# Performance work log

Measured on AMD Instinct MI355X. Metric: run time of the kernel, lower is better.

## Reference

```python
import jax, jax.numpy as jnp
import numpy as np

B, S, HIDDEN, H, HD = 4, 1024, 1024, 16, 64  # head_dim = hidden/heads; rel-pos 'd_model' = HD
TABLE = 2 * HD - 1  # 127


def setup_inputs() -> dict:
    key = jax.random.key(0)
    ks = jax.random.split(key, 16)
    sc = 0.02
    return {
        "query": jax.random.normal(ks[0], (B, S, HIDDEN), jnp.float32),
        "key": jax.random.normal(ks[1], (B, S, HIDDEN), jnp.float32),
        "value": jax.random.normal(ks[2], (B, S, HIDDEN), jnp.float32),
        "Wq": jax.random.normal(ks[3], (H, HIDDEN, HD), jnp.float32) * sc,
        "Wk": jax.random.normal(ks[4], (H, HIDDEN, HD), jnp.float32) * sc,
        "Wv": jax.random.normal(ks[5], (H, HIDDEN, HD), jnp.float32) * sc,
        "bq": jax.random.normal(ks[6], (H, HD), jnp.float32) * sc,
        "bk": jax.random.normal(ks[7], (H, HD), jnp.float32) * sc,
        "bv": jax.random.normal(ks[8], (H, HD), jnp.float32) * sc,
        "rp_k_table": jax.random.normal(ks[9], (TABLE, HD), jnp.float32) * sc,
        "rp_v_table": jax.random.normal(ks[10], (TABLE, HD), jnp.float32) * sc,
        "Wfc": jax.random.normal(ks[11], (HIDDEN, HIDDEN), jnp.float32) * sc,
        "bfc": jax.random.normal(ks[12], (HIDDEN,), jnp.float32) * sc,
    }


def _rel_bias(table, length, hd):
    # distance clipped to [-(hd-1), hd-1], shifted -> index into (2*hd-1, hd) table
    i = jnp.arange(length)
    idx = jnp.clip(i[None, :] - i[:, None], -(hd - 1), hd - 1) + (hd - 1)
    return table[idx]  # [S, S, hd]


def reference(query, key, value, Wq, Wk, Wv, bq, bk, bv, rp_k_table, rp_v_table, Wfc, bfc):
    hd = Wq.shape[-1]
    b, s, _ = query.shape
    k_bias = _rel_bias(rp_k_table, s, hd)  # [S,S,hd], shared across heads
    v_bias = _rel_bias(rp_v_table, s, hd)
    # per-head projections: [B,H,S,hd]
    q = jnp.einsum('bsh,nhd->bnsd', query, Wq) + bq[None, :, None, :]
    kk = jnp.einsum('bsh,nhd->bnsd', key, Wk) + bk[None, :, None, :]
    v = jnp.einsum('bsh,nhd->bnsd', value, Wv) + bv[None, :, None, :]
    # scores: QK^T plus Shaw-style relative-position key bias
    scores = (jnp.einsum('bnid,bnjd->bnij', q, kk)
              + jnp.einsum('bnid,ijd->bnij', q, k_bias)) / (hd ** 0.5)
    w = jax.nn.softmax(scores, axis=-1)  # [B,H,S,S]
    out = (jnp.einsum('bnij,bnjd->bnid', w, v)
           + jnp.einsum('bnij,ijd->bnid', w, v_bias))  # [B,H,S,hd]
    hidden = out.transpose(0, 2, 1, 3).reshape(b, s, -1)  # concat heads
    return hidden @ Wfc.T + bfc
```

## Files before the change

### kernel.cpp

```cpp
#include <hip/hip_runtime.h>
#include <stdint.h>

typedef unsigned int u32;
typedef unsigned short u16;
typedef float f32x4 __attribute__((ext_vector_type(4)));
typedef __bf16 bfx8 __attribute__((ext_vector_type(8)));
typedef short s16x8 __attribute__((ext_vector_type(8)));
typedef short s16x4 __attribute__((ext_vector_type(4)));
typedef int i32x4 __attribute__((ext_vector_type(4)));

#define DEVI static __device__ __forceinline__


DEVI u16 f2bf(float f){
  u32 u = __builtin_bit_cast(u32, f);
  u32 r = (u + 0x7fffu + ((u >> 16) & 1u)) >> 16;
  return (u16)r;
}

DEVI f32x4 mfma16(s16x8 a, s16x8 b, f32x4 c){
  return __builtin_amdgcn_mfma_f32_16x16x32_bf16(
      __builtin_bit_cast(bfx8, a), __builtin_bit_cast(bfx8, b), c, 0, 0, 0);
}

DEVI void gld16(const void* g, void* l){
  __builtin_amdgcn_global_load_lds(
      (__attribute__((address_space(1))) void*)g,
      (__attribute__((address_space(3))) void*)l, 16, 0, 0);
}

__global__ void cast3_kernel(const float* __restrict__ a, const float* __restrict__ b,
                             const float* __restrict__ c, u16* __restrict__ dst){
  const long n_each = 4194304;
  long stride = (long)gridDim.x * blockDim.x;
  for (long v = (long)blockIdx.x * blockDim.x + threadIdx.x; v < 3 * n_each / 8; v += stride){
    long idx8 = v * 8;
    int which = (int)(idx8 / n_each);
    long off = idx8 - (long)which * n_each;
    const float* s = which == 0 ? a : (which == 1 ? b : c);
    float4 f0 = *(const float4*)(s + off);
    float4 f1 = *(const float4*)(s + off + 4);
    s16x8 o;
    o[0]=(short)f2bf(f0.x); o[1]=(short)f2bf(f0.y); o[2]=(short)f2bf(f0.z); o[3]=(short)f2bf(f0.w);
    o[4]=(short)f2bf(f1.x); o[5]=(short)f2bf(f1.y); o[6]=(short)f2bf(f1.z); o[7]=(short)f2bf(f1.w);
    *(s16x8*)(dst + idx8) = o;
  }
}

__global__ void cast1_kernel(const float* __restrict__ a, u16* __restrict__ dst, long n){
  long stride = (long)gridDim.x * blockDim.x;
  for (long v = (long)blockIdx.x * blockDim.x + threadIdx.x; v < n / 8; v += stride){
    long idx8 = v * 8;
    float4 f0 = *(const float4*)(a + idx8);
    float4 f1 = *(const float4*)(a + idx8 + 4);
    s16x8 o;
    o[0]=(short)f2bf(f0.x); o[1]=(short)f2bf(f0.y); o[2]=(short)f2bf(f0.z); o[3]=(short)f2bf(f0.w);
    o[4]=(short)f2bf(f1.x); o[5]=(short)f2bf(f1.y); o[6]=(short)f2bf(f1.z); o[7]=(short)f2bf(f1.w);
    *(s16x8*)(dst + idx8) = o;
  }
}

__global__ void wtrans_kernel(const float* __restrict__ Wq, const float* __restrict__ Wk,
                              const float* __restrict__ Wv, u16* __restrict__ Wt){
  int bid = blockIdx.x;
  int kt = bid & 15; int h = (bid >> 4) & 15; int proj = bid >> 8;
  const float* W = (proj == 0 ? Wq : (proj == 1 ? Wk : Wv)) + (long)h * (1024 * 64);
  __shared__ u16 lt[64][66];
  int t = threadIdx.x;
  #pragma unroll
  for (int it = 0; it < 16; ++it){
    int idx = it * 256 + t;
    int r = idx >> 6, d = idx & 63;
    lt[r][d] = f2bf(W[(long)(kt * 64 + r) * 64 + d]);
  }
  __syncthreads();
  long outbase = (long)proj * 1024 + h * 64;
  #pragma unroll
  for (int it = 0; it < 16; ++it){
    int idx = it * 256 + t;
    int d = idx >> 6, r = idx & 63;
    Wt[(outbase + d) * 1024 + kt * 64 + r] = lt[r][d];
  }
}

__global__ void tables_kernel(const float* __restrict__ rpk, const float* __restrict__ rpv,
                              u16* __restrict__ rpkb, u16* __restrict__ rpvT){
  int t = threadIdx.x;
  for (int i = t; i < 128 * 64; i += 256){
    int row = i >> 6, d = i & 63;
    rpkb[i] = (row < 127) ? f2bf(rpk[row * 64 + d]) : (u16)0;
  }
  for (int i = t; i < 64 * 128; i += 256){
    int d = i >> 7, row = i & 127;
    rpvT[i] = (row < 127) ? f2bf(rpv[row * 64 + d]) : (u16)0;
  }
}

__global__ void vtrans_kernel(const u16* __restrict__ Vb, u16* __restrict__ Vt){
  int bid = blockIdx.x;
  int st = bid & 15, bh = bid >> 4;
  const u16* src = Vb + ((long)bh * 1024 + st * 64) * 64;
  u16* dst = Vt + (long)bh * 64 * 1024 + st * 64;
  __shared__ u16 lt[64][66];
  int t = threadIdx.x;
  #pragma unroll
  for (int it = 0; it < 16; ++it){
    int idx = it * 256 + t;
    int r = idx >> 6, d = idx & 63;
    lt[r][d] = src[idx];
  }
  __syncthreads();
  #pragma unroll
  for (int it = 0; it < 16; ++it){
    int idx = it * 256 + t;
    int d = idx >> 6, r = idx & 63;
    dst[(long)d * 1024 + r] = lt[r][d];
  }
}

DEVI void gemm_core(const u16* __restrict__ A, const u16* __restrict__ Bt,
                    int m0, int n0, u16* lds, int tid, f32x4 (&acc)[4][4]){
  const int K = 1024;
  int w = tid >> 6, lane = tid & 63, g = lane >> 4, li = lane & 15;
  int wm = w >> 1, wn = w & 1;
  for (int ks = 0; ks < 16; ++ks){
    int k0 = ks * 64;
    __syncthreads();
    #pragma unroll
    for (int i = 0; i < 4; ++i){
      int c = i * 256 + w * 64 + lane;
      int r = c >> 3, s = lane & 7;
      int kk = k0 + ((s ^ (r & 7)) << 3);
      gld16(A + (long)(m0 + r) * K + kk, (char*)lds + (i * 256 + w * 64) * 16);
      gld16(Bt + (long)(n0 + r) * K + kk, (char*)lds + 16384 + (i * 256 + w * 64) * 16);
    }
    __syncthreads();
    #pragma unroll
    for (int kh = 0; kh < 2; ++kh){
      s16x8 af[4], bfr[4];
      #pragma unroll
      for (int mi = 0; mi < 4; ++mi){
        int row = wm * 64 + mi * 16 + li;
        int byt = (row * 128 + (kh * 32 + g * 8) * 2) ^ ((li & 7) << 4);
        af[mi] = *(const s16x8*)((const char*)lds + byt);
      }
      #pragma unroll
      for (int ni = 0; ni < 4; ++ni){
        int row = wn * 64 + ni * 16 + li;
        int byt = 16384 + ((row * 128 + (kh * 32 + g * 8) * 2) ^ ((li & 7) << 4));
        bfr[ni] = *(const s16x8*)((const char*)lds + byt);
      }
      #pragma unroll
      for (int mi = 0; mi < 4; ++mi)
        #pragma unroll
        for (int ni = 0; ni < 4; ++ni)
          acc[mi][ni] = mfma16(af[mi], bfr[ni], acc[mi][ni]);
    }
  }
}

__launch_bounds__(256, 2)
__global__ void gemm_qkv(const u16* __restrict__ Xb, const u16* __restrict__ Wt,
                         const float* __restrict__ bq, const float* __restrict__ bk,
                         const float* __restrict__ bv,
                         u16* __restrict__ Qb, u16* __restrict__ Kb, u16* __restrict__ Vb){
  __shared__ __align__(16) u16 lds[16384];
  int tid = threadIdx.x;
  int bidx = blockIdx.x;
  int bn = bidx % 24, bm = bidx / 24;
  int m0 = bm * 128, n0 = bn * 128;
  int proj = n0 >> 10;
  const u16* A = Xb + (long)proj * 4096 * 1024;
  f32x4 acc[4][4] = {};
  gemm_core(A, Wt, m0, n0, lds, tid, acc);
  int w = tid >> 6, lane = tid & 63, g = lane >> 4, li = lane & 15;
  int wm = w >> 1, wn = w & 1;
  const float* bias = proj == 0 ? bq : (proj == 1 ? bk : bv);
  u16* Dst = proj == 0 ? Qb : (proj == 1 ? Kb : Vb);
  float scale = (proj == 0) ? 0.125f : 1.0f;
  #pragma unroll
  for (int mi = 0; mi < 4; ++mi)
    #pragma unroll
    for (int ni = 0; ni < 4; ++ni)
      #pragma unroll
      for (int r = 0; r < 4; ++r){
        int m = m0 + wm * 64 + mi * 16 + g * 4 + r;
        int n = n0 + wn * 64 + ni * 16 + li;
        int nn = n & 1023;
        float v = (acc[mi][ni][r] + bias[nn]) * scale;
        int b = m >> 10, s = m & 1023;
        int h = nn >> 6, d = nn & 63;
        Dst[((long)(b * 16 + h) * 1024 + s) * 64 + d] = f2bf(v);
      }
}

__launch_bounds__(256, 2)
__global__ void gemm_fc(const u16* __restrict__ Hid, const u16* __restrict__ Wfcb,
                        const float* __restrict__ bfc, float* __restrict__ out){
  __shared__ __align__(16) u16 lds[16384];
  int tid = threadIdx.x;
  int bidx = blockIdx.x;
  int bn = bidx & 7, bm = bidx >> 3;
  int m0 = bm * 128, n0 = bn * 128;
  f32x4 acc[4][4] = {};
  gemm_core(Hid, Wfcb, m0, n0, lds, tid, acc);
  int w = tid >> 6, lane = tid & 63, g = lane >> 4, li = lane & 15;
  int wm = w >> 1, wn = w & 1;
  #pragma unroll
  for (int mi = 0; mi < 4; ++mi)
    #pragma unroll
    for (int ni = 0; ni < 4; ++ni)
      #pragma unroll
      for (int r = 0; r < 4; ++r){
        int m = m0 + wm * 64 + mi * 16 + g * 4 + r;
        int n = n0 + wn * 64 + ni * 16 + li;
        out[(long)m * 1024 + n] = acc[mi][ni][r] + bfc[n];
      }
}

__launch_bounds__(256, 2)
__global__ void attn_kernel(const u16* __restrict__ Qb, const u16* __restrict__ Kb,
                            const u16* __restrict__ Vt, const u16* __restrict__ rpkb,
                            const u16* __restrict__ rpvT, u16* __restrict__ Hid){
  const int S = 1024;
  int bh = blockIdx.y;
  int i0 = blockIdx.x * 64;
  int bb = bh >> 4, hh = bh & 15;
  const u16* Qp = Qb + (long)bh * S * 64;
  const u16* Kp = Kb + (long)bh * S * 64;
  const u16* Vp = Vt + (long)bh * 64 * S;
  int tid = threadIdx.x, w = tid >> 6, lane = tid & 63, g = lane >> 4, li = lane & 15;

  __shared__ __align__(16) float rq[64 * 128];
  __shared__ __align__(16) u16 bw[64 * 128];
  __shared__ float redL[4][64], redR[4][64], redD[4][64];

  s16x8 qf[4][2];
  #pragma unroll
  for (int ni = 0; ni < 4; ++ni)
    #pragma unroll
    for (int kh = 0; kh < 2; ++kh)
      qf[ni][kh] = *(const s16x8*)(Qp + (long)(i0 + ni * 16 + li) * 64 + kh * 32 + g * 8);

  {
    i32x4 z = {0, 0, 0, 0};
    #pragma unroll
    for (int i = 0; i < 4; ++i) ((i32x4*)bw)[i * 256 + tid] = z;
  }

  #pragma unroll
  for (int tt = 0; tt < 2; ++tt){
    int tb = w * 2 + tt;
    s16x8 pf0 = *(const s16x8*)(rpkb + (tb * 16 + li) * 64 + g * 8);
    s16x8 pf1 = *(const s16x8*)(rpkb + (tb * 16 + li) * 64 + 32 + g * 8);
    #pragma unroll
    for (int ni = 0; ni < 4; ++ni){
      f32x4 r = {0.f, 0.f, 0.f, 0.f};
      r = mfma16(qf[ni][0], pf0, r);
      r = mfma16(qf[ni][1], pf1, r);
      #pragma unroll
      for (int e = 0; e < 4; ++e)
        rq[(ni * 16 + g * 4 + e) * 128 + tb * 16 + li] = r[e];
    }
  }
  __syncthreads();

  f32x4 oacc[4][4] = {};
  float dacc[4] = {0, 0, 0, 0}, Lac[4] = {0, 0, 0, 0}, Rac[4] = {0, 0, 0, 0};

  for (int jt = 0; jt < 8; ++jt){
    int jw = jt * 128 + w * 32;
    s16x8 kf[2][2];
    #pragma unroll
    for (int mi = 0; mi < 2; ++mi)
      #pragma unroll
      for (int kh = 0; kh < 2; ++kh)
        kf[mi][kh] = *(const s16x8*)(Kp + (long)(jw + mi * 16 + li) * 64 + kh * 32 + g * 8);
    s16x8 av[4];
    #pragma unroll
    for (int mi = 0; mi < 2; ++mi){
      f32x4 sacc[4];
      #pragma unroll
      for (int ni = 0; ni < 4; ++ni){
        f32x4 s0 = {0.f, 0.f, 0.f, 0.f};
        s0 = mfma16(kf[mi][0], qf[ni][0], s0);
        s0 = mfma16(kf[mi][1], qf[ni][1], s0);
        sacc[ni] = s0;
      }
      #pragma unroll
      for (int ni = 0; ni < 4; ++ni){
        int iloc = ni * 16 + li;
        #pragma unroll
        for (int r = 0; r < 4; ++r){
          int jgl = jw + mi * 16 + g * 4 + r;
          int delta = jgl - (i0 + iloc);
          int t = delta < -63 ? 0 : (delta > 63 ? 126 : delta + 63);
          float sv = sacc[ni][r] + rq[iloc * 128 + t];
          float e = __expf(sv);
          dacc[ni] += e;
          u16 eb = f2bf(e);
          av[ni][mi * 4 + r] = (short)eb;
          if (delta >= -62 && delta <= 62){
            int byt = (iloc * 256 + (delta + 63) * 2) ^ ((iloc & 7) << 4);
            *(u16*)((char*)bw + byt) = eb;
          } else if (delta <= -63){
            Lac[ni] += e;
          } else {
            Rac[ni] += e;
          }
        }
      }
    }
    #pragma unroll
    for (int nd = 0; nd < 4; ++nd){
      const u16* vp = Vp + (long)(nd * 16 + li) * S + jw + g * 4;
      s16x4 vlo = *(const s16x4*)(vp);
      s16x4 vhi = *(const s16x4*)(vp + 16);
      s16x8 vv;
      vv[0]=vlo[0]; vv[1]=vlo[1]; vv[2]=vlo[2]; vv[3]=vlo[3];
      vv[4]=vhi[0]; vv[5]=vhi[1]; vv[6]=vhi[2]; vv[7]=vhi[3];
      #pragma unroll
      for (int ni = 0; ni < 4; ++ni)
        oacc[ni][nd] = mfma16(av[ni], vv, oacc[ni][nd]);
    }
  }

  #pragma unroll
  for (int ni = 0; ni < 4; ++ni){
    dacc[ni] += __shfl_xor(dacc[ni], 16); dacc[ni] += __shfl_xor(dacc[ni], 32);
    Lac[ni]  += __shfl_xor(Lac[ni], 16);  Lac[ni]  += __shfl_xor(Lac[ni], 32);
    Rac[ni]  += __shfl_xor(Rac[ni], 16);  Rac[ni]  += __shfl_xor(Rac[ni], 32);
  }
  if (g == 0){
    #pragma unroll
    for (int ni = 0; ni < 4; ++ni){
      redL[w][ni * 16 + li] = Lac[ni];
      redR[w][ni * 16 + li] = Rac[ni];
      redD[w][ni * 16 + li] = dacc[ni];
    }
  }
  __syncthreads();
  if (tid < 64){
    int i = tid;
    float Ls = redL[0][i] + redL[1][i] + redL[2][i] + redL[3][i];
    float Rs = redR[0][i] + redR[1][i] + redR[2][i] + redR[3][i];
    float Ds = redD[0][i] + redD[1][i] + redD[2][i] + redD[3][i];
    *(u16*)((char*)bw + ((i * 256 + 0)   ^ ((i & 7) << 4))) = f2bf(Ls);
    *(u16*)((char*)bw + ((i * 256 + 252) ^ ((i & 7) << 4))) = f2bf(Rs);
    redD[0][i] = Ds;
  }
  float* Ored = rq;
  for (int ww = 0; ww < 4; ++ww){
    if (w == ww){
      #pragma unroll
      for (int ni = 0; ni < 4; ++ni)
        #pragma unroll
        for (int nd = 0; nd < 4; ++nd)
          #pragma unroll
          for (int r = 0; r < 4; ++r){
            int i = ni * 16 + g * 4 + r, d = nd * 16 + li;
            if (ww == 0) Ored[i * 64 + d] = oacc[ni][nd][r];
            else         Ored[i * 64 + d] += oacc[ni][nd][r];
          }
    }
    __syncthreads();
  }
  s16x8 rvf[4];
  #pragma unroll
  for (int ksl = 0; ksl < 4; ++ksl)
    rvf[ksl] = *(const s16x8*)(rpvT + (w * 16 + li) * 128 + ksl * 32 + g * 8);
  f32x4 bacc[4];
  #pragma unroll
  for (int mi = 0; mi < 4; ++mi){
    f32x4 a4 = {0.f, 0.f, 0.f, 0.f};
    #pragma unroll
    for (int ksl = 0; ksl < 4; ++ksl){
      int row = mi * 16 + li;
      int byt = (row * 256 + (ksl * 32 + g * 8) * 2) ^ ((row & 7) << 4);
      s16x8 a = *(const s16x8*)((const char*)bw + byt);
      a4 = mfma16(a, rvf[ksl], a4);
    }
    bacc[mi] = a4;
  }
  #pragma unroll
  for (int mi = 0; mi < 4; ++mi)
    #pragma unroll
    for (int r = 0; r < 4; ++r){
      int i = mi * 16 + g * 4 + r;
      float den = redD[0][i];
      float o = (Ored[i * 64 + w * 16 + li] + bacc[mi][r]) / den;
      Hid[((long)bb * S + i0 + i) * 1024 + hh * 64 + w * 16 + li] = f2bf(o);
    }
}

extern "C" void kernel_launch(void* const* d_in, const int* in_sizes, int n_in,
                              void* d_out, int out_size, void* d_ws, size_t ws_size,
                              hipStream_t stream){
  const float* query = (const float*)d_in[0];
  const float* key   = (const float*)d_in[1];
  const float* value = (const float*)d_in[2];
  const float* Wq  = (const float*)d_in[3];
  const float* Wk  = (const float*)d_in[4];
  const float* Wv  = (const float*)d_in[5];
  const float* bq  = (const float*)d_in[6];
  const float* bk  = (const float*)d_in[7];
  const float* bv  = (const float*)d_in[8];
  const float* rpk = (const float*)d_in[9];
  const float* rpv = (const float*)d_in[10];
  const float* Wfc = (const float*)d_in[11];
  const float* bfc = (const float*)d_in[12];
  float* out = (float*)d_out;

  u16* Xb   = (u16*)d_ws;
  u16* Wt   = Xb + 3L * 4096 * 1024;
  u16* Wfcb = Wt + 3072L * 1024;
  u16* rpkb = Wfcb + 1024L * 1024;
  u16* rpvT = rpkb + 128 * 64;
  u16* Qb   = rpvT + 64 * 128;
  u16* Kb   = Qb + 64L * 1024 * 64;
  u16* Vb   = Kb + 64L * 1024 * 64;
  u16* Vt   = Vb + 64L * 1024 * 64;
  u16* Hid  = Vt + 64L * 1024 * 64;

  cast3_kernel<<<2048, 256, 0, stream>>>(query, key, value, Xb);
  cast1_kernel<<<512, 256, 0, stream>>>(Wfc, Wfcb, 1024L * 1024);
  wtrans_kernel<<<768, 256, 0, stream>>>(Wq, Wk, Wv, Wt);
  tables_kernel<<<1, 256, 0, stream>>>(rpk, rpv, rpkb, rpvT);
  gemm_qkv<<<768, 256, 0, stream>>>(Xb, Wt, bq, bk, bv, Qb, Kb, Vb);
  vtrans_kernel<<<1024, 256, 0, stream>>>(Vb, Vt);
  attn_kernel<<<dim3(16, 64), 256, 0, stream>>>(Qb, Kb, Vt, rpkb, rpvT, Hid);
  gemm_fc<<<256, 256, 0, stream>>>(Hid, Wfcb, bfc, out);
}
```

Baseline: 304.5 us.

## Skip per-element rel-pos work on far tiles, use exp2 and shrink attention LDS

```diff
diff --git a/kernel.cpp b/kernel.cpp
--- a/kernel.cpp
+++ b/kernel.cpp
@@ -11,12 +11,19 @@
 
 #define DEVI static __device__ __forceinline__
 
+#if __has_builtin(__builtin_amdgcn_exp2f)
+#define EXP2(x) __builtin_amdgcn_exp2f(x)
+#else
+#define EXP2(x) exp2f(x)
+#endif
+
 
 DEVI u16 f2bf(float f){
   u32 u = __builtin_bit_cast(u32, f);
   u32 r = (u + 0x7fffu + ((u >> 16) & 1u)) >> 16;
   return (u16)r;
 }
+DEVI float b2f(u16 v){ return __builtin_bit_cast(float, (u32)v << 16); }
 
 DEVI f32x4 mfma16(s16x8 a, s16x8 b, f32x4 c){
   return __builtin_amdgcn_mfma_f32_16x16x32_bf16(
@@ -166,7 +173,8 @@
                          u16* __restrict__ Qb, u16* __restrict__ Kb, u16* __restrict__ Vb){
   __shared__ __align__(16) u16 lds[16384];
   int tid = threadIdx.x;
-  int bidx = blockIdx.x;
+  int bo = blockIdx.x;
+  int bidx = (bo & 7) * 96 + (bo >> 3);
   int bn = bidx % 24, bm = bidx / 24;
   int m0 = bm * 128, n0 = bn * 128;
   int proj = n0 >> 10;
@@ -177,7 +185,7 @@
   int wm = w >> 1, wn = w & 1;
   const float* bias = proj == 0 ? bq : (proj == 1 ? bk : bv);
   u16* Dst = proj == 0 ? Qb : (proj == 1 ? Kb : Vb);
-  float scale = (proj == 0) ? 0.125f : 1.0f;
+  float scale = (proj == 0) ? 0.125f * 1.44269504f : 1.0f;
   #pragma unroll
   for (int mi = 0; mi < 4; ++mi)
     #pragma unroll
@@ -218,7 +226,7 @@
       }
 }
 
-__launch_bounds__(256, 2)
+__launch_bounds__(256, 4)
 __global__ void attn_kernel(const u16* __restrict__ Qb, const u16* __restrict__ Kb,
                             const u16* __restrict__ Vt, const u16* __restrict__ rpkb,
                             const u16* __restrict__ rpvT, u16* __restrict__ Hid){
@@ -231,9 +239,13 @@
   const u16* Vp = Vt + (long)bh * 64 * S;
   int tid = threadIdx.x, w = tid >> 6, lane = tid & 63, g = lane >> 4, li = lane & 15;
 
-  __shared__ __align__(16) float rq[64 * 128];
-  __shared__ __align__(16) u16 bw[64 * 128];
-  __shared__ float redL[4][64], redR[4][64], redD[4][64];
+  __shared__ __align__(16) char smem[35840];
+  u16* rqb  = (u16*)smem;
+  u16* bw   = (u16*)(smem + 16384);
+  float* redL = (float*)(smem + 32768);
+  float* redR = redL + 256;
+  float* redD = redR + 256;
+  float* Ored = (float*)smem;
 
   s16x8 qf[4][2];
   #pragma unroll
@@ -260,10 +272,18 @@
       r = mfma16(qf[ni][1], pf1, r);
       #pragma unroll
       for (int e = 0; e < 4; ++e)
-        rq[(ni * 16 + g * 4 + e) * 128 + tb * 16 + li] = r[e];
+        rqb[(ni * 16 + g * 4 + e) * 128 + tb * 16 + li] = f2bf(r[e]);
     }
   }
   __syncthreads();
+
+  float rqL[4], rqR[4];
+  #pragma unroll
+  for (int ni = 0; ni < 4; ++ni){
+    int iloc = ni * 16 + li;
+    rqL[ni] = b2f(rqb[iloc * 128]);
+    rqR[ni] = b2f(rqb[iloc * 128 + 126]);
+  }
 
   f32x4 oacc[4][4] = {};
   float dacc[4] = {0, 0, 0, 0}, Lac[4] = {0, 0, 0, 0}, Rac[4] = {0, 0, 0, 0};
@@ -279,6 +299,7 @@
     s16x8 av[4];
     #pragma unroll
     for (int mi = 0; mi < 2; ++mi){
+      int js0 = jw + mi * 16;
       f32x4 sacc[4];
       #pragma unroll
       for (int ni = 0; ni < 4; ++ni){
@@ -287,26 +308,47 @@
         s0 = mfma16(kf[mi][1], qf[ni][1], s0);
         sacc[ni] = s0;
       }
-      #pragma unroll
-      for (int ni = 0; ni < 4; ++ni){
-        int iloc = ni * 16 + li;
+      if (js0 >= i0 + 126){
         #pragma unroll
-        for (int r = 0; r < 4; ++r){
-          int jgl = jw + mi * 16 + g * 4 + r;
-          int delta = jgl - (i0 + iloc);
-          int t = delta < -63 ? 0 : (delta > 63 ? 126 : delta + 63);
-          float sv = sacc[ni][r] + rq[iloc * 128 + t];
-          float e = __expf(sv);
-          dacc[ni] += e;
-          u16 eb = f2bf(e);
-          av[ni][mi * 4 + r] = (short)eb;
-          if (delta >= -62 && delta <= 62){
-            int byt = (iloc * 256 + (delta + 63) * 2) ^ ((iloc & 7) << 4);
-            *(u16*)((char*)bw + byt) = eb;
-          } else if (delta <= -63){
-            Lac[ni] += e;
-          } else {
-            Rac[ni] += e;
+        for (int ni = 0; ni < 4; ++ni)
+          #pragma unroll
+          for (int r = 0; r < 4; ++r){
+            float e = EXP2(sacc[ni][r] + rqR[ni]);
+            dacc[ni] += e; Rac[ni] += e;
+            av[ni][mi * 4 + r] = (short)f2bf(e);
+          }
+      } else if (js0 + 78 <= i0){
+        #pragma unroll
+        for (int ni = 0; ni < 4; ++ni)
+          #pragma unroll
+          for (int r = 0; r < 4; ++r){
+            float e = EXP2(sacc[ni][r] + rqL[ni]);
+            dacc[ni] += e; Lac[ni] += e;
+            av[ni][mi * 4 + r] = (short)f2bf(e);
+          }
+      } else {
+        #pragma unroll
+        for (int ni = 0; ni < 4; ++ni){
+          int iloc = ni * 16 + li;
+          #pragma unroll
+          for (int r = 0; r < 4; ++r){
+            int jgl = js0 + g * 4 + r;
+            int delta = jgl - (i0 + iloc);
+            int dcl = delta < -62 ? -62 : (delta > 62 ? 62 : delta);
+            int tg = dcl + 63;
+            float rqv = b2f(rqb[iloc * 128 + tg]);
+            bool lft = delta < -62, rgt = delta > 62;
+            rqv = lft ? rqL[ni] : (rgt ? rqR[ni] : rqv);
+            float e = EXP2(sacc[ni][r] + rqv);
+            dacc[ni] += e;
+            u16 eb = f2bf(e);
+            av[ni][mi * 4 + r] = (short)eb;
+            if (!lft && !rgt){
+              int byt = (iloc * 256 + tg * 2) ^ ((iloc & 7) << 4);
+              *(u16*)((char*)bw + byt) = eb;
+            }
+            Lac[ni] += lft ? e : 0.f;
+            Rac[ni] += rgt ? e : 0.f;
           }
         }
       }
@@ -334,22 +376,21 @@
   if (g == 0){
     #pragma unroll
     for (int ni = 0; ni < 4; ++ni){
-      redL[w][ni * 16 + li] = Lac[ni];
-      redR[w][ni * 16 + li] = Rac[ni];
-      redD[w][ni * 16 + li] = dacc[ni];
+      redL[w * 64 + ni * 16 + li] = Lac[ni];
+      redR[w * 64 + ni * 16 + li] = Rac[ni];
+      redD[w * 64 + ni * 16 + li] = dacc[ni];
     }
   }
   __syncthreads();
   if (tid < 64){
     int i = tid;
-    float Ls = redL[0][i] + redL[1][i] + redL[2][i] + redL[3][i];
-    float Rs = redR[0][i] + redR[1][i] + redR[2][i] + redR[3][i];
-    float Ds = redD[0][i] + redD[1][i] + redD[2][i] + redD[3][i];
+    float Ls = redL[i] + redL[64 + i] + redL[128 + i] + redL[192 + i];
+    float Rs = redR[i] + redR[64 + i] + redR[128 + i] + redR[192 + i];
+    float Ds = redD[i] + redD[64 + i] + redD[128 + i] + redD[192 + i];
     *(u16*)((char*)bw + ((i * 256 + 0)   ^ ((i & 7) << 4))) = f2bf(Ls);
     *(u16*)((char*)bw + ((i * 256 + 252) ^ ((i & 7) << 4))) = f2bf(Rs);
-    redD[0][i] = Ds;
-  }
-  float* Ored = rq;
+    redD[i] = Ds;
+  }
   for (int ww = 0; ww < 4; ++ww){
     if (w == ww){
       #pragma unroll
@@ -387,7 +428,7 @@
     #pragma unroll
     for (int r = 0; r < 4; ++r){
       int i = mi * 16 + g * 4 + r;
-      float den = redD[0][i];
+      float den = redD[i];
       float o = (Ored[i * 64 + w * 16 + li] + bacc[mi][r]) / den;
       Hid[((long)bb * S + i0 + i) * 1024 + hh * 64 + w * 16 + li] = f2bf(o);
     }
```

After: 391.4 us. 1.29x slower.

## Split attention rows across waves and specialise far-diagonal blocks with exp2

Applied to the files above, without the earlier changes.

```diff
diff --git a/kernel.cpp b/kernel.cpp
--- a/kernel.cpp
+++ b/kernel.cpp
@@ -11,12 +11,23 @@
 
 #define DEVI static __device__ __forceinline__
 
+#if __has_builtin(__builtin_amdgcn_exp2f)
+#define EXP2(x) __builtin_amdgcn_exp2f(x)
+#else
+#define EXP2(x) exp2f(x)
+#endif
+
 
 DEVI u16 f2bf(float f){
   u32 u = __builtin_bit_cast(u32, f);
   u32 r = (u + 0x7fffu + ((u >> 16) & 1u)) >> 16;
   return (u16)r;
 }
+DEVI float b2f(u16 v){ return __builtin_bit_cast(float, (u32)v << 16); }
+DEVI short e2s(float f){ return __builtin_bit_cast(short, (__bf16)f); }
+
+struct s16x4p { s16x4 lo, hi; };
+DEVI s16x8 cat4(s16x4 lo, s16x4 hi){ s16x4p p{lo, hi}; return __builtin_bit_cast(s16x8, p); }
 
 DEVI f32x4 mfma16(s16x8 a, s16x8 b, f32x4 c){
   return __builtin_amdgcn_mfma_f32_16x16x32_bf16(
@@ -166,7 +177,8 @@
                          u16* __restrict__ Qb, u16* __restrict__ Kb, u16* __restrict__ Vb){
   __shared__ __align__(16) u16 lds[16384];
   int tid = threadIdx.x;
-  int bidx = blockIdx.x;
+  int bo = blockIdx.x;
+  int bidx = (bo & 7) * 96 + (bo >> 3);
   int bn = bidx % 24, bm = bidx / 24;
   int m0 = bm * 128, n0 = bn * 128;
   int proj = n0 >> 10;
@@ -177,7 +189,7 @@
   int wm = w >> 1, wn = w & 1;
   const float* bias = proj == 0 ? bq : (proj == 1 ? bk : bv);
   u16* Dst = proj == 0 ? Qb : (proj == 1 ? Kb : Vb);
-  float scale = (proj == 0) ? 0.125f : 1.0f;
+  float scale = (proj == 0) ? 0.125f * 1.44269504f : 1.0f;
   #pragma unroll
   for (int mi = 0; mi < 4; ++mi)
     #pragma unroll
@@ -230,166 +242,133 @@
   const u16* Kp = Kb + (long)bh * S * 64;
   const u16* Vp = Vt + (long)bh * 64 * S;
   int tid = threadIdx.x, w = tid >> 6, lane = tid & 63, g = lane >> 4, li = lane & 15;
-
-  __shared__ __align__(16) float rq[64 * 128];
-  __shared__ __align__(16) u16 bw[64 * 128];
-  __shared__ float redL[4][64], redR[4][64], redD[4][64];
-
-  s16x8 qf[4][2];
-  #pragma unroll
-  for (int ni = 0; ni < 4; ++ni)
-    #pragma unroll
-    for (int kh = 0; kh < 2; ++kh)
-      qf[ni][kh] = *(const s16x8*)(Qp + (long)(i0 + ni * 16 + li) * 64 + kh * 32 + g * 8);
+  int gi0 = i0 + w * 16;
+
+  __shared__ __align__(16) u16 rqb[64 * 128];
+  __shared__ __align__(16) u16 bwb[64 * 128];
+
+  s16x8 qf[2];
+  #pragma unroll
+  for (int kh = 0; kh < 2; ++kh)
+    qf[kh] = *(const s16x8*)(Qp + (long)(gi0 + li) * 64 + kh * 32 + g * 8);
 
   {
     i32x4 z = {0, 0, 0, 0};
-    #pragma unroll
-    for (int i = 0; i < 4; ++i) ((i32x4*)bw)[i * 256 + tid] = z;
-  }
-
-  #pragma unroll
-  for (int tt = 0; tt < 2; ++tt){
-    int tb = w * 2 + tt;
+    i32x4* bz = (i32x4*)(bwb + w * 16 * 128);
+    #pragma unroll
+    for (int zz = 0; zz < 4; ++zz) bz[zz * 64 + lane] = z;
+  }
+
+  #pragma unroll
+  for (int tb = 0; tb < 8; ++tb){
     s16x8 pf0 = *(const s16x8*)(rpkb + (tb * 16 + li) * 64 + g * 8);
     s16x8 pf1 = *(const s16x8*)(rpkb + (tb * 16 + li) * 64 + 32 + g * 8);
-    #pragma unroll
-    for (int ni = 0; ni < 4; ++ni){
-      f32x4 r = {0.f, 0.f, 0.f, 0.f};
-      r = mfma16(qf[ni][0], pf0, r);
-      r = mfma16(qf[ni][1], pf1, r);
-      #pragma unroll
-      for (int e = 0; e < 4; ++e)
-        rq[(ni * 16 + g * 4 + e) * 128 + tb * 16 + li] = r[e];
-    }
-  }
-  __syncthreads();
-
-  f32x4 oacc[4][4] = {};
-  float dacc[4] = {0, 0, 0, 0}, Lac[4] = {0, 0, 0, 0}, Rac[4] = {0, 0, 0, 0};
-
-  for (int jt = 0; jt < 8; ++jt){
-    int jw = jt * 128 + w * 32;
+    f32x4 r = {0.f, 0.f, 0.f, 0.f};
+    r = mfma16(qf[0], pf0, r);
+    r = mfma16(qf[1], pf1, r);
+    #pragma unroll
+    for (int e = 0; e < 4; ++e)
+      rqb[(w * 16 + g * 4 + e) * 128 + tb * 16 + li] = f2bf(r[e]);
+  }
+
+  float rqL = b2f(rqb[(w * 16 + li) * 128]);
+  float rqR = b2f(rqb[(w * 16 + li) * 128 + 126]);
+
+  f32x4 oacc[4] = {};
+  float dacc = 0.f, Lac = 0.f, Rac = 0.f;
+
+  for (int js = 0; js < 64; js += 2){
+    int jb = js * 16;
     s16x8 kf[2][2];
     #pragma unroll
-    for (int mi = 0; mi < 2; ++mi)
+    for (int p = 0; p < 2; ++p)
       #pragma unroll
       for (int kh = 0; kh < 2; ++kh)
-        kf[mi][kh] = *(const s16x8*)(Kp + (long)(jw + mi * 16 + li) * 64 + kh * 32 + g * 8);
-    s16x8 av[4];
-    #pragma unroll
-    for (int mi = 0; mi < 2; ++mi){
-      f32x4 sacc[4];
-      #pragma unroll
-      for (int ni = 0; ni < 4; ++ni){
-        f32x4 s0 = {0.f, 0.f, 0.f, 0.f};
-        s0 = mfma16(kf[mi][0], qf[ni][0], s0);
-        s0 = mfma16(kf[mi][1], qf[ni][1], s0);
-        sacc[ni] = s0;
-      }
-      #pragma unroll
-      for (int ni = 0; ni < 4; ++ni){
-        int iloc = ni * 16 + li;
+        kf[p][kh] = *(const s16x8*)(Kp + (long)(jb + p * 16 + li) * 64 + kh * 32 + g * 8);
+    s16x8 vv[4];
+    #pragma unroll
+    for (int nd = 0; nd < 4; ++nd){
+      const u16* vp = Vp + (long)(nd * 16 + li) * S + jb + g * 4;
+      vv[nd] = cat4(*(const s16x4*)(vp), *(const s16x4*)(vp + 16));
+    }
+    s16x8 av;
+    #pragma unroll
+    for (int p = 0; p < 2; ++p){
+      int js0 = jb + p * 16;
+      f32x4 sacc = {0.f, 0.f, 0.f, 0.f};
+      sacc = mfma16(kf[p][0], qf[0], sacc);
+      sacc = mfma16(kf[p][1], qf[1], sacc);
+      if (js0 >= gi0 + 78){
         #pragma unroll
         for (int r = 0; r < 4; ++r){
-          int jgl = jw + mi * 16 + g * 4 + r;
-          int delta = jgl - (i0 + iloc);
-          int t = delta < -63 ? 0 : (delta > 63 ? 126 : delta + 63);
-          float sv = sacc[ni][r] + rq[iloc * 128 + t];
-          float e = __expf(sv);
-          dacc[ni] += e;
-          u16 eb = f2bf(e);
-          av[ni][mi * 4 + r] = (short)eb;
-          if (delta >= -62 && delta <= 62){
-            int byt = (iloc * 256 + (delta + 63) * 2) ^ ((iloc & 7) << 4);
-            *(u16*)((char*)bw + byt) = eb;
-          } else if (delta <= -63){
-            Lac[ni] += e;
-          } else {
-            Rac[ni] += e;
+          float e = EXP2(sacc[r] + rqR);
+          Rac += e;
+          av[p * 4 + r] = e2s(e);
+        }
+      } else if (js0 + 78 <= gi0){
+        #pragma unroll
+        for (int r = 0; r < 4; ++r){
+          float e = EXP2(sacc[r] + rqL);
+          Lac += e;
+          av[p * 4 + r] = e2s(e);
+        }
+      } else {
+        #pragma unroll
+        for (int r = 0; r < 4; ++r){
+          int jgl = js0 + g * 4 + r;
+          int delta = jgl - (gi0 + li);
+          int dcl = delta < -62 ? -62 : (delta > 62 ? 62 : delta);
+          int tg = dcl + 63;
+          float rqv = b2f(rqb[(w * 16 + li) * 128 + tg]);
+          bool lft = delta < -62, rgt = delta > 62;
+          rqv = lft ? rqL : (rgt ? rqR : rqv);
+          float e = EXP2(sacc[r] + rqv);
+          short eb = e2s(e);
+          av[p * 4 + r] = eb;
+          if (!lft && !rgt){
+            int byt = ((w * 16 + li) * 256 + tg * 2) ^ ((li & 7) << 4);
+            *(u16*)((char*)bwb + byt) = (u16)eb;
+            dacc += e;
           }
+          Lac += lft ? e : 0.f;
+          Rac += rgt ? e : 0.f;
         }
       }
     }
     #pragma unroll
+    for (int nd = 0; nd < 4; ++nd)
+      oacc[nd] = mfma16(av, vv[nd], oacc[nd]);
+  }
+
+  dacc += __shfl_xor(dacc, 16); dacc += __shfl_xor(dacc, 32);
+  Lac  += __shfl_xor(Lac, 16);  Lac  += __shfl_xor(Lac, 32);
+  Rac  += __shfl_xor(Rac, 16);  Rac  += __shfl_xor(Rac, 32);
+  float Dtot = dacc + Lac + Rac;
+  if (g == 0){
+    *(u16*)((char*)bwb + (((w * 16 + li) * 256 + 0)   ^ ((li & 7) << 4))) = f2bf(Lac);
+    *(u16*)((char*)bwb + (((w * 16 + li) * 256 + 252) ^ ((li & 7) << 4))) = f2bf(Rac);
+  }
+  f32x4 bacc[4] = {};
+  #pragma unroll
+  for (int ksl = 0; ksl < 4; ++ksl){
+    int byt = (((w * 16 + li) * 256) + (ksl * 32 + g * 8) * 2) ^ ((li & 7) << 4);
+    s16x8 a = *(const s16x8*)((const char*)bwb + byt);
+    #pragma unroll
     for (int nd = 0; nd < 4; ++nd){
-      const u16* vp = Vp + (long)(nd * 16 + li) * S + jw + g * 4;
-      s16x4 vlo = *(const s16x4*)(vp);
-      s16x4 vhi = *(const s16x4*)(vp + 16);
-      s16x8 vv;
-      vv[0]=vlo[0]; vv[1]=vlo[1]; vv[2]=vlo[2]; vv[3]=vlo[3];
-      vv[4]=vhi[0]; vv[5]=vhi[1]; vv[6]=vhi[2]; vv[7]=vhi[3];
-      #pragma unroll
-      for (int ni = 0; ni < 4; ++ni)
-        oacc[ni][nd] = mfma16(av[ni], vv, oacc[ni][nd]);
-    }
-  }
-
-  #pragma unroll
-  for (int ni = 0; ni < 4; ++ni){
-    dacc[ni] += __shfl_xor(dacc[ni], 16); dacc[ni] += __shfl_xor(dacc[ni], 32);
-    Lac[ni]  += __shfl_xor(Lac[ni], 16);  Lac[ni]  += __shfl_xor(Lac[ni], 32);
-    Rac[ni]  += __shfl_xor(Rac[ni], 16);  Rac[ni]  += __shfl_xor(Rac[ni], 32);
-  }
-  if (g == 0){
-    #pragma unroll
-    for (int ni = 0; ni < 4; ++ni){
-      redL[w][ni * 16 + li] = Lac[ni];
-      redR[w][ni * 16 + li] = Rac[ni];
-      redD[w][ni * 16 + li] = dacc[ni];
-    }
-  }
-  __syncthreads();
-  if (tid < 64){
-    int i = tid;
-    float Ls = redL[0][i] + redL[1][i] + redL[2][i] + redL[3][i];
-    float Rs = redR[0][i] + redR[1][i] + redR[2][i] + redR[3][i];
-    float Ds = redD[0][i] + redD[1][i] + redD[2][i] + redD[3][i];
-    *(u16*)((char*)bw + ((i * 256 + 0)   ^ ((i & 7) << 4))) = f2bf(Ls);
-    *(u16*)((char*)bw + ((i * 256 + 252) ^ ((i & 7) << 4))) = f2bf(Rs);
-    redD[0][i] = Ds;
-  }
-  float* Ored = rq;
-  for (int ww = 0; ww < 4; ++ww){
-    if (w == ww){
-      #pragma unroll
-      for (int ni = 0; ni < 4; ++ni)
-        #pragma unroll
-        for (int nd = 0; nd < 4; ++nd)
-          #pragma unroll
-          for (int r = 0; r < 4; ++r){
-            int i = ni * 16 + g * 4 + r, d = nd * 16 + li;
-            if (ww == 0) Ored[i * 64 + d] = oacc[ni][nd][r];
-            else         Ored[i * 64 + d] += oacc[ni][nd][r];
-          }
-    }
-    __syncthreads();
-  }
-  s16x8 rvf[4];
-  #pragma unroll
-  for (int ksl = 0; ksl < 4; ++ksl)
-    rvf[ksl] = *(const s16x8*)(rpvT + (w * 16 + li) * 128 + ksl * 32 + g * 8);
-  f32x4 bacc[4];
-  #pragma unroll
-  for (int mi = 0; mi < 4; ++mi){
-    f32x4 a4 = {0.f, 0.f, 0.f, 0.f};
-    #pragma unroll
-    for (int ksl = 0; ksl < 4; ++ksl){
-      int row = mi * 16 + li;
-      int byt = (row * 256 + (ksl * 32 + g * 8) * 2) ^ ((row & 7) << 4);
-      s16x8 a = *(const s16x8*)((const char*)bw + byt);
-      a4 = mfma16(a, rvf[ksl], a4);
-    }
-    bacc[mi] = a4;
-  }
-  #pragma unroll
-  for (int mi = 0; mi < 4; ++mi)
+      s16x8 rv = *(const s16x8*)(rpvT + (nd * 16 + li) * 128 + ksl * 32 + g * 8);
+      bacc[nd] = mfma16(a, rv, bacc[nd]);
+    }
+  }
+  float inv[4];
+  #pragma unroll
+  for (int r = 0; r < 4; ++r)
+    inv[r] = 1.0f / __shfl(Dtot, g * 4 + r);
+  #pragma unroll
+  for (int nd = 0; nd < 4; ++nd)
     #pragma unroll
     for (int r = 0; r < 4; ++r){
-      int i = mi * 16 + g * 4 + r;
-      float den = redD[0][i];
-      float o = (Ored[i * 64 + w * 16 + li] + bacc[mi][r]) / den;
-      Hid[((long)bb * S + i0 + i) * 1024 + hh * 64 + w * 16 + li] = f2bf(o);
+      float o = (oacc[nd][r] + bacc[nd][r]) * inv[r];
+      Hid[((long)bb * S + gi0 + g * 4 + r) * 1024 + hh * 64 + nd * 16 + li] = f2bf(o);
     }
 }
 
```

Measured after the change: 383.2 us. 25.8% more time.
